# Performance work log

Hardware: AMD Instinct MI355X
Metric: run time of the kernel (lower is better)

Reference implementation:

```python
import jax, jax.numpy as jnp
import numpy as np

HID = 1024     # hidden_dim
HEADS = 8      # num_heads
HD = HID // HEADS  # head_dim = 128
MD = 8         # manifold_dim
L = 3          # num_layers
B, S = 8, 1024
EPS = 1e-7
BALL_MAX = 1.0 - 1e-5  # clamp inside Poincare ball (|curvature| = 1)


def expmap0(v):
    """Hyperbolic exponential map at origin, curvature -1 (Poincare ball)."""
    n = jnp.sqrt(jnp.sum(v * v, axis=-1, keepdims=True))
    n = jnp.maximum(n, EPS)
    return jnp.tanh(n) * v / n


def logmap0(y):
    """Hyperbolic logarithm map at origin, curvature -1 (Poincare ball)."""
    n = jnp.sqrt(jnp.sum(y * y, axis=-1, keepdims=True))
    n_c = jnp.clip(n, EPS, BALL_MAX)
    return jnp.arctanh(n_c) * y / n_c


def setup_inputs() -> dict:
    key = jax.random.key(0)
    ks = jax.random.split(key, 6)
    sc = 0.02
    return {
        "x": jax.random.normal(ks[0], (B, S, HID), dtype=jnp.float32),
        "W_qkv": jax.random.normal(ks[1], (HID, 3 * HID), dtype=jnp.float32) * sc,
        "b_qkv": jnp.zeros((3 * HID,), dtype=jnp.float32),
        "W_pinv": jax.random.normal(ks[2], (HID, MD), dtype=jnp.float32) * sc,
        "b_pinv": jnp.zeros((MD,), dtype=jnp.float32),
        "W_attn": jax.random.normal(ks[3], (L, MD, HID), dtype=jnp.float32) * sc,
        "b_attn": jnp.zeros((L, HID), dtype=jnp.float32),
        "W_out": jax.random.normal(ks[4], (HID, HID), dtype=jnp.float32) * sc,
        "b_out": jnp.zeros((HID,), dtype=jnp.float32),
    }


def reference(x, W_qkv, b_qkv, W_pinv, b_pinv, W_attn, b_attn, W_out, b_out):
    inv_sqrt_d = 1.0 / np.sqrt(HD).astype(np.float32)
    cur = x
    for l in range(L):
        qkv = jnp.einsum('bsh,hd->bsd', cur, W_qkv) + b_qkv  # [B,S,3*HID]
        q, k, v = jnp.split(qkv, 3, axis=-1)
        # [B,S,HID] -> [B,HEADS,S,HD]
        def heads(t):
            return t.reshape(B, S, HEADS, HD).transpose(0, 2, 1, 3)
        q, k, v = heads(q), heads(k), heads(v)
        # geometric 'flow': hyperbolic retraction of Q/K onto the Poincare ball
        # (parallel transport at the origin is identity)
        qf = expmap0(q)
        kf = expmap0(k)
        scores = jnp.einsum('bhqd,bhkd->bhqk', qf, kf) * inv_sqrt_d
        att = jax.nn.softmax(scores, axis=-1)
        o = jnp.einsum('bhqk,bhkd->bhqd', att, v)  # [B,H,S,HD]
        o = o.transpose(0, 2, 1, 3).reshape(B, S, HID)
        # project to manifold coords, then per-layer pattern projection back
        m = jnp.einsum('bsh,hm->bsm', o, W_pinv) + b_pinv           # [B,S,MD]
        upd = jnp.einsum('bsm,mh->bsh', m, W_attn[l]) + b_attn[l]   # [B,S,HID]
        cur = cur + upd
    return jnp.einsum('bsh,hd->bsd', cur, W_out) + b_out
```

## Files before the change

### kernel.cpp

```cpp
#include <hip/hip_runtime.h>
#include <hip/hip_bf16.h>
#include <hip/hip_fp8.h>
#include <cstdint>

typedef __hip_bfloat16 bf16;
typedef __bf16 b8 __attribute__((ext_vector_type(8)));
typedef float f4v __attribute__((ext_vector_type(4)));
typedef short s8v __attribute__((ext_vector_type(8)));
typedef int i8v __attribute__((ext_vector_type(8)));

#define DEVI static __device__ __forceinline__

DEVI void gload16(const void* g, void* l) {
  __builtin_amdgcn_global_load_lds(
      (const __attribute__((address_space(1))) void*)(uintptr_t)g,
      (__attribute__((address_space(3))) void*)(uint32_t)(uintptr_t)l,
      16, 0, 0);
}

DEVI f4v mfma_bf16(b8 a, b8 b, f4v c) {
  return __builtin_amdgcn_mfma_f32_16x16x32_bf16(a, b, c, 0, 0, 0);
}

DEVI f4v mfma_fp8(i8v a, i8v b, f4v c) {
  return __builtin_amdgcn_mfma_scale_f32_16x16x128_f8f6f4(
      a, b, c, 0, 0, 0, 0x7F7F7F7F, 0, 0x7F7F7F7F);
}

DEVI uint8_t to_fp8(float f) {
  __hip_fp8_e4m3 v(f);
  return v.__x;
}

__global__ void prep_kernel(const float* __restrict__ x, float* __restrict__ cur,
                            bf16* __restrict__ curb, uint8_t* __restrict__ curf8) {
  int i = (blockIdx.x * 256 + threadIdx.x) * 4;
  float4 v = *(const float4*)(x + i);
  *(float4*)(cur + i) = v;
  __hip_bfloat162 a, b;
  a.x = __float2bfloat16(v.x); a.y = __float2bfloat16(v.y);
  b.x = __float2bfloat16(v.z); b.y = __float2bfloat16(v.w);
  *(__hip_bfloat162*)(curb + i) = a;
  *(__hip_bfloat162*)(curb + i + 2) = b;
  uint32_t p = (uint32_t)to_fp8(v.x) | ((uint32_t)to_fp8(v.y) << 8) |
               ((uint32_t)to_fp8(v.z) << 16) | ((uint32_t)to_fp8(v.w) << 24);
  *(uint32_t*)(curf8 + i) = p;
}

__global__ void transpose_cast(const float* __restrict__ in, bf16* __restrict__ out,
                               int R, int C) {
  __shared__ float tile[32][33];
  int c0 = blockIdx.x * 32, r0 = blockIdx.y * 32;
  int tx = threadIdx.x & 31, ty = threadIdx.x >> 5;
  for (int rr = ty; rr < 32; rr += 8)
    tile[rr][tx] = in[(size_t)(r0 + rr) * C + c0 + tx];
  __syncthreads();
  for (int cc = ty; cc < 32; cc += 8)
    out[(size_t)(c0 + cc) * R + r0 + tx] = __float2bfloat16(tile[tx][cc]);
}

__global__ void transpose_cast_fp8(const float* __restrict__ in,
                                   uint8_t* __restrict__ out, int R, int C) {
  __shared__ float tile[32][33];
  int c0 = blockIdx.x * 32, r0 = blockIdx.y * 32;
  int tx = threadIdx.x & 31, ty = threadIdx.x >> 5;
  for (int rr = ty; rr < 32; rr += 8)
    tile[rr][tx] = in[(size_t)(r0 + rr) * C + c0 + tx];
  __syncthreads();
  for (int cc = ty; cc < 32; cc += 8)
    out[(size_t)(c0 + cc) * R + r0 + tx] = to_fp8(tile[tx][cc]);
}

__global__ __launch_bounds__(256, 3)
void gemm_qkv_fp8(const uint8_t* __restrict__ A, const uint8_t* __restrict__ Bt,
                  const float* __restrict__ bias, bf16* __restrict__ Qo,
                  bf16* __restrict__ Ko, bf16* __restrict__ Vto, int M, int N,
                  int K) {
  __shared__ uint8_t As[128 * 128];
  __shared__ uint8_t Bs[128 * 128];
  __shared__ float red[2][128];
  const int t = threadIdx.x;
  const int w = t >> 6, lane = t & 63;
  const int lm = lane & 15, qd = lane >> 4;
  const int m0 = blockIdx.x * 128, n0 = blockIdx.y * 128;
  const int wm = (w & 1) * 64, wn = (w >> 1) * 64;

  const uint8_t* Ag = A + (size_t)m0 * K;
  const uint8_t* Bg = Bt + (size_t)n0 * K;

  f4v acc[4][4];
  f4v zero = {0.f, 0.f, 0.f, 0.f};
#pragma unroll
  for (int i = 0; i < 4; i++)
#pragma unroll
    for (int j = 0; j < 4; j++) acc[i][j] = zero;

  for (int k0 = 0; k0 < K; k0 += 128) {
#pragma unroll
    for (int c = 0; c < 4; c++) {
      int s = c * 256 + t;
      int r = s >> 3;
      int kc = (s & 7) ^ (r & 7);
      gload16(Ag + (size_t)r * K + k0 + kc * 16, &As[s * 16]);
      gload16(Bg + (size_t)r * K + k0 + kc * 16, &Bs[s * 16]);
    }
    __syncthreads();
    i8v af[4], bfr[4];
#pragma unroll
    for (int tm = 0; tm < 4; tm++) {
      int row = wm + tm * 16 + lm;
      int ch = (qd * 2) ^ (row & 7);
      union { int4 q[2]; i8v v; } u;
      u.q[0] = *(const int4*)&As[row * 128 + ch * 16];
      u.q[1] = *(const int4*)&As[row * 128 + (ch ^ 1) * 16];
      af[tm] = u.v;
    }
#pragma unroll
    for (int tn = 0; tn < 4; tn++) {
      int row = wn + tn * 16 + lm;
      int ch = (qd * 2) ^ (row & 7);
      union { int4 q[2]; i8v v; } u;
      u.q[0] = *(const int4*)&Bs[row * 128 + ch * 16];
      u.q[1] = *(const int4*)&Bs[row * 128 + (ch ^ 1) * 16];
      bfr[tn] = u.v;
    }
    __builtin_amdgcn_s_setprio(1);
#pragma unroll
    for (int tm = 0; tm < 4; tm++)
#pragma unroll
      for (int tn = 0; tn < 4; tn++)
        acc[tm][tn] = mfma_fp8(af[tm], bfr[tn], acc[tm][tn]);
    __builtin_amdgcn_s_setprio(0);
    __syncthreads();
  }

  const int part = n0 >> 10;
  const int hh = (n0 >> 7) & 7;
  if (part == 2) {
#pragma unroll
    for (int tm = 0; tm < 4; tm++)
#pragma unroll
      for (int tn = 0; tn < 4; tn++) {
        int d = wn + tn * 16 + lm;
        float bv = bias[n0 + d];
        int row0 = m0 + wm + tm * 16 + qd * 4;
        int b = row0 >> 10, s0 = row0 & 1023;
        bf16 vt[4];
#pragma unroll
        for (int r = 0; r < 4; r++) vt[r] = __float2bfloat16(acc[tm][tn][r] + bv);
        *(ushort4*)&Vto[((size_t)(b * 8 + hh)) * 131072 + (size_t)d * 1024 + s0] =
            *(ushort4*)vt;
      }
  } else {
    float bvs[4];
#pragma unroll
    for (int tn = 0; tn < 4; tn++) bvs[tn] = bias[n0 + wn + tn * 16 + lm];
    float ss[4][4];
#pragma unroll
    for (int tm = 0; tm < 4; tm++)
#pragma unroll
      for (int r = 0; r < 4; r++) {
        float s = 0.f;
#pragma unroll
        for (int tn = 0; tn < 4; tn++) {
          float v = acc[tm][tn][r] + bvs[tn];
          s += v * v;
        }
#pragma unroll
        for (int off = 1; off < 16; off <<= 1) s += __shfl_xor(s, off, 64);
        ss[tm][r] = s;
      }
    if (lm == 0) {
#pragma unroll
      for (int tm = 0; tm < 4; tm++)
#pragma unroll
        for (int r = 0; r < 4; r++)
          red[w >> 1][wm + tm * 16 + qd * 4 + r] = ss[tm][r];
    }
    __syncthreads();
    const float qsc = (part == 0) ? 0.08838834764831845f : 1.0f;
    float scr[4][4];
#pragma unroll
    for (int tm = 0; tm < 4; tm++)
#pragma unroll
      for (int r = 0; r < 4; r++) {
        int row = wm + tm * 16 + qd * 4 + r;
        float tot = red[0][row] + red[1][row];
        float nrm = fmaxf(sqrtf(tot), 1e-7f);
        scr[tm][r] = tanhf(nrm) / nrm * qsc;
      }
    bf16* dst = (part == 0) ? Qo : Ko;
#pragma unroll
    for (int tm = 0; tm < 4; tm++)
#pragma unroll
      for (int tn = 0; tn < 4; tn++) {
        int d = wn + tn * 16 + lm;
        int row0 = m0 + wm + tm * 16 + qd * 4;
        int b = row0 >> 10, s0 = row0 & 1023;
#pragma unroll
        for (int r = 0; r < 4; r++)
          dst[(((size_t)(b * 8 + hh)) * 1024 + s0 + r) * 128 + d] =
              __float2bfloat16((acc[tm][tn][r] + bvs[tn]) * scr[tm][r]);
      }
  }
}

__global__ __launch_bounds__(256, 3)
void gemm_bt(const bf16* __restrict__ A, const bf16* __restrict__ Bt,
             const float* __restrict__ bias, float* __restrict__ Cf, int M, int N,
             int K) {
  __shared__ bf16 As[128 * 64];
  __shared__ bf16 Bs[128 * 64];
  const int t = threadIdx.x;
  const int w = t >> 6, lane = t & 63;
  const int lm = lane & 15, qd = lane >> 4;
  const int m0 = blockIdx.x * 128, n0 = blockIdx.y * 128;
  const int wm = (w & 1) * 64, wn = (w >> 1) * 64;

  const bf16* Ag = A + (size_t)m0 * K;
  const bf16* Bg = Bt + (size_t)n0 * K;

  f4v acc[4][4];
  f4v zero = {0.f, 0.f, 0.f, 0.f};
#pragma unroll
  for (int i = 0; i < 4; i++)
#pragma unroll
    for (int j = 0; j < 4; j++) acc[i][j] = zero;

  for (int k0 = 0; k0 < K; k0 += 64) {
#pragma unroll
    for (int c = 0; c < 4; c++) {
      int s = c * 256 + t;
      int r = s >> 3;
      int kc = (s & 7) ^ (r & 7);
      gload16(Ag + (size_t)r * K + k0 + kc * 8, &As[s * 8]);
      gload16(Bg + (size_t)r * K + k0 + kc * 8, &Bs[s * 8]);
    }
    __syncthreads();
#pragma unroll
    for (int ks = 0; ks < 2; ks++) {
      b8 af[4], bfr[4];
#pragma unroll
      for (int tm = 0; tm < 4; tm++) {
        int row = wm + tm * 16 + lm;
        int ch = (ks * 4 + qd) ^ (row & 7);
        af[tm] = *(const b8*)&As[row * 64 + ch * 8];
      }
#pragma unroll
      for (int tn = 0; tn < 4; tn++) {
        int row = wn + tn * 16 + lm;
        int ch = (ks * 4 + qd) ^ (row & 7);
        bfr[tn] = *(const b8*)&Bs[row * 64 + ch * 8];
      }
      __builtin_amdgcn_s_setprio(1);
#pragma unroll
      for (int tm = 0; tm < 4; tm++)
#pragma unroll
        for (int tn = 0; tn < 4; tn++)
          acc[tm][tn] = mfma_bf16(af[tm], bfr[tn], acc[tm][tn]);
      __builtin_amdgcn_s_setprio(0);
    }
    __syncthreads();
  }

#pragma unroll
  for (int tm = 0; tm < 4; tm++)
#pragma unroll
    for (int tn = 0; tn < 4; tn++) {
      int col = n0 + wn + tn * 16 + lm;
      float bv = bias[col];
#pragma unroll
      for (int r = 0; r < 4; r++) {
        int row = m0 + wm + tm * 16 + qd * 4 + r;
        Cf[(size_t)row * N + col] = acc[tm][tn][r] + bv;
      }
    }
}

__global__ __launch_bounds__(256, 2)
void attn_kernel(const bf16* __restrict__ Qf, const bf16* __restrict__ Kf,
                 const bf16* __restrict__ Vt, const float* __restrict__ Wpinv,
                 float* __restrict__ Mpart) {
  __shared__ bf16 smem[40960];
  bf16* Ps = smem + 32768;
  const int t = threadIdx.x, w = t >> 6, lane = t & 63;
  const int lm = lane & 15, qd = lane >> 4;
  const int bh = blockIdx.x, qt = blockIdx.y;
  const bf16* Qg = Qf + ((size_t)bh * 1024 + qt * 128) * 128;
  const bf16* Kg = Kf + (size_t)bh * 131072;
  const bf16* Vg = Vt + (size_t)bh * 131072;
  bf16* Pw = Ps + w * 2048;

  auto stage = [&](int kt, int b) {
    bf16* Ksb = smem + b * 16384;
    bf16* Vsb = Ksb + 8192;
#pragma unroll
    for (int c = 0; c < 4; c++) {
      int s = c * 256 + t;
      int r = s >> 4;
      int kc = (s & 15) ^ (r & 7);
      gload16(Kg + (size_t)(kt * 64 + r) * 128 + kc * 8, &Ksb[s * 8]);
      int rv = s >> 3;
      int kv = (s & 7) ^ (rv & 7);
      gload16(Vg + (size_t)rv * 1024 + kt * 64 + kv * 8, &Vsb[s * 8]);
    }
  };

  b8 qfr[2][4];
#pragma unroll
  for (int mt = 0; mt < 2; mt++)
#pragma unroll
    for (int ks = 0; ks < 4; ks++)
      qfr[mt][ks] =
          *(const b8*)(Qg + (size_t)(w * 32 + mt * 16 + lm) * 128 + ks * 32 + qd * 8);

  f4v o[2][8];
  f4v lacc[2];
  f4v zero = {0.f, 0.f, 0.f, 0.f};
#pragma unroll
  for (int mt = 0; mt < 2; mt++) {
    lacc[mt] = zero;
#pragma unroll
    for (int i = 0; i < 8; i++) o[mt][i] = zero;
  }
  union { s8v s; b8 b; } uo;
#pragma unroll
  for (int i = 0; i < 8; i++) uo.s[i] = 0x3F80;
  const b8 ones = uo.b;

  stage(0, 0);
  for (int kt = 0; kt < 16; kt++) {
    const int cb = kt & 1;
    if (kt < 15) {
      stage(kt + 1, cb ^ 1);
      asm volatile("s_waitcnt vmcnt(8)" ::: "memory");
    } else {
      asm volatile("s_waitcnt vmcnt(0)" ::: "memory");
    }
    __builtin_amdgcn_sched_barrier(0);
    __builtin_amdgcn_s_barrier();
    __builtin_amdgcn_sched_barrier(0);
    const bf16* Ks = smem + cb * 16384;
    const bf16* Vs = Ks + 8192;

    f4v sc[2][4];
#pragma unroll
    for (int mt = 0; mt < 2; mt++)
#pragma unroll
      for (int tn = 0; tn < 4; tn++) sc[mt][tn] = zero;
    __builtin_amdgcn_s_setprio(1);
#pragma unroll
    for (int tn = 0; tn < 4; tn++) {
      int krow = tn * 16 + lm;
#pragma unroll
      for (int ks = 0; ks < 4; ks++) {
        int ch = (ks * 4 + qd) ^ (krow & 7);
        b8 kfr = *(const b8*)&Ks[krow * 128 + ch * 8];
        sc[0][tn] = mfma_bf16(qfr[0][ks], kfr, sc[0][tn]);
        sc[1][tn] = mfma_bf16(qfr[1][ks], kfr, sc[1][tn]);
      }
    }
    __builtin_amdgcn_s_setprio(0);
#pragma unroll
    for (int mt = 0; mt < 2; mt++)
#pragma unroll
      for (int tn = 0; tn < 4; tn++)
#pragma unroll
        for (int r = 0; r < 4; r++) {
          int qi = mt * 16 + qd * 4 + r;
          int ch = (tn * 2 + (lm >> 3)) ^ ((qi >> 1) & 7);
          Pw[qi * 64 + ch * 8 + (lm & 7)] = __float2bfloat16(__expf(sc[mt][tn][r]));
        }

    b8 pa[2][2];
#pragma unroll
    for (int mt = 0; mt < 2; mt++)
#pragma unroll
      for (int kv2 = 0; kv2 < 2; kv2++) {
        int qi = mt * 16 + lm;
        int ch = (kv2 * 4 + qd) ^ ((lm >> 1) & 7);
        pa[mt][kv2] = *(const b8*)&Pw[qi * 64 + ch * 8];
      }
    __builtin_amdgcn_s_setprio(1);
#pragma unroll
    for (int mt = 0; mt < 2; mt++)
#pragma unroll
      for (int kv2 = 0; kv2 < 2; kv2++)
        lacc[mt] = mfma_bf16(pa[mt][kv2], ones, lacc[mt]);
#pragma unroll
    for (int tnd = 0; tnd < 8; tnd++) {
      int drow = tnd * 16 + lm;
#pragma unroll
      for (int kv2 = 0; kv2 < 2; kv2++) {
        int ch = (kv2 * 4 + qd) ^ (drow & 7);
        b8 vfr = *(const b8*)&Vs[drow * 64 + ch * 8];
#pragma unroll
        for (int mt = 0; mt < 2; mt++)
          o[mt][tnd] = mfma_bf16(pa[mt][kv2], vfr, o[mt][tnd]);
      }
    }
    __builtin_amdgcn_s_setprio(0);
    __builtin_amdgcn_sched_barrier(0);
    __builtin_amdgcn_s_barrier();
  }

  const int h = bh & 7;
  float wp[8][8];
#pragma unroll
  for (int tnd = 0; tnd < 8; tnd++) {
    const float* wr = Wpinv + (size_t)(h * 128 + tnd * 16 + lm) * 8;
    float4 wa = *(const float4*)wr;
    float4 wb = *(const float4*)(wr + 4);
    wp[tnd][0] = wa.x; wp[tnd][1] = wa.y; wp[tnd][2] = wa.z; wp[tnd][3] = wa.w;
    wp[tnd][4] = wb.x; wp[tnd][5] = wb.y; wp[tnd][6] = wb.z; wp[tnd][7] = wb.w;
  }
#pragma unroll
  for (int mt = 0; mt < 2; mt++) {
    float rinv[4];
#pragma unroll
    for (int r = 0; r < 4; r++) rinv[r] = 1.0f / lacc[mt][r];
#pragma unroll
    for (int r = 0; r < 4; r++) {
      float pm[8];
#pragma unroll
      for (int j = 0; j < 8; j++) pm[j] = 0.f;
#pragma unroll
      for (int tnd = 0; tnd < 8; tnd++) {
        float ov = o[mt][tnd][r] * rinv[r];
#pragma unroll
        for (int j = 0; j < 8; j++) pm[j] += ov * wp[tnd][j];
      }
#pragma unroll
      for (int j = 0; j < 8; j++) {
#pragma unroll
        for (int off = 1; off < 16; off <<= 1)
          pm[j] += __shfl_xor(pm[j], off, 64);
      }
      float sv = pm[0];
#pragma unroll
      for (int j = 1; j < 8; j++) sv = (lm == j) ? pm[j] : sv;
      if (lm < 8) {
        int sIdx = qt * 128 + w * 32 + mt * 16 + qd * 4 + r;
        Mpart[((size_t)bh * 1024 + sIdx) * 8 + lm] = sv;
      }
    }
  }
}

__global__ __launch_bounds__(256, 4)
void update_kernel(const float* __restrict__ Mpart, const float* __restrict__ bpinv,
                   const float* __restrict__ Wattn, const float* __restrict__ battn,
                   float* __restrict__ cur, bf16* __restrict__ curb,
                   uint8_t* __restrict__ curf8) {
  const int t = threadIdx.x, w = t >> 6, lane = t & 63;
  const int r0 = blockIdx.x * 8 + w * 2;
  const int hb = lane * 4;
  const int hh = lane >> 3, jj = lane & 7;

  float a0[8], a1[8];
  {
    const int b0 = r0 >> 10, s0 = r0 & 1023;
    float v0 = Mpart[(((size_t)b0 * 8 + hh) * 1024 + s0) * 8 + jj];
    float v1 = Mpart[(((size_t)b0 * 8 + hh) * 1024 + s0 + 1) * 8 + jj];
#pragma unroll
    for (int off = 8; off < 64; off <<= 1) {
      v0 += __shfl_xor(v0, off, 64);
      v1 += __shfl_xor(v1, off, 64);
    }
#pragma unroll
    for (int j = 0; j < 8; j++) {
      float bp = bpinv[j];
      a0[j] = __shfl(v0, j, 64) + bp;
      a1[j] = __shfl(v1, j, 64) + bp;
    }
  }

#pragma unroll
  for (int c = 0; c < 4; c++) {
    float4 bv = *(const float4*)(battn + c * 256 + hb);
    float u00 = bv.x, u01 = bv.y, u02 = bv.z, u03 = bv.w;
    float u10 = bv.x, u11 = bv.y, u12 = bv.z, u13 = bv.w;
#pragma unroll
    for (int j = 0; j < 8; j++) {
      float4 wv = *(const float4*)(Wattn + (size_t)j * 1024 + c * 256 + hb);
      u00 += a0[j] * wv.x; u01 += a0[j] * wv.y;
      u02 += a0[j] * wv.z; u03 += a0[j] * wv.w;
      u10 += a1[j] * wv.x; u11 += a1[j] * wv.y;
      u12 += a1[j] * wv.z; u13 += a1[j] * wv.w;
    }
    {
      float* cp = cur + (size_t)r0 * 1024 + c * 256 + hb;
      float4 c4 = *(float4*)cp;
      c4.x += u00; c4.y += u01; c4.z += u02; c4.w += u03;
      *(float4*)cp = c4;
      bf16 cb[4];
      cb[0] = __float2bfloat16(c4.x); cb[1] = __float2bfloat16(c4.y);
      cb[2] = __float2bfloat16(c4.z); cb[3] = __float2bfloat16(c4.w);
      *(ushort4*)(curb + (size_t)r0 * 1024 + c * 256 + hb) = *(ushort4*)cb;
      uint32_t p = (uint32_t)to_fp8(c4.x) | ((uint32_t)to_fp8(c4.y) << 8) |
                   ((uint32_t)to_fp8(c4.z) << 16) | ((uint32_t)to_fp8(c4.w) << 24);
      *(uint32_t*)(curf8 + (size_t)r0 * 1024 + c * 256 + hb) = p;
    }
    {
      float* cp = cur + (size_t)(r0 + 1) * 1024 + c * 256 + hb;
      float4 c4 = *(float4*)cp;
      c4.x += u10; c4.y += u11; c4.z += u12; c4.w += u13;
      *(float4*)cp = c4;
      bf16 cb[4];
      cb[0] = __float2bfloat16(c4.x); cb[1] = __float2bfloat16(c4.y);
      cb[2] = __float2bfloat16(c4.z); cb[3] = __float2bfloat16(c4.w);
      *(ushort4*)(curb + (size_t)(r0 + 1) * 1024 + c * 256 + hb) = *(ushort4*)cb;
      uint32_t p = (uint32_t)to_fp8(c4.x) | ((uint32_t)to_fp8(c4.y) << 8) |
                   ((uint32_t)to_fp8(c4.z) << 16) | ((uint32_t)to_fp8(c4.w) << 24);
      *(uint32_t*)(curf8 + (size_t)(r0 + 1) * 1024 + c * 256 + hb) = p;
    }
  }
}

extern "C" void kernel_launch(void* const* d_in, const int* in_sizes, int n_in,
                              void* d_out, int out_size, void* d_ws, size_t ws_size,
                              hipStream_t stream) {
  const float* x      = (const float*)d_in[0];
  const float* W_qkv  = (const float*)d_in[1];
  const float* b_qkv  = (const float*)d_in[2];
  const float* W_pinv = (const float*)d_in[3];
  const float* b_pinv = (const float*)d_in[4];
  const float* W_attn = (const float*)d_in[5];
  const float* b_attn = (const float*)d_in[6];
  const float* W_out  = (const float*)d_in[7];
  const float* b_out  = (const float*)d_in[8];

  char* ws = (char*)d_ws;
  size_t off = 0;
  auto alloc = [&](size_t bytes) -> void* {
    void* p = ws + off;
    off += (bytes + 255) & ~(size_t)255;
    return p;
  };
  float* cur     = (float*)alloc((size_t)8192 * 1024 * 4);
  bf16* curb     = (bf16*)alloc((size_t)8192 * 1024 * 2);
  uint8_t* curf8 = (uint8_t*)alloc((size_t)8192 * 1024);
  uint8_t* Wqkv8 = (uint8_t*)alloc((size_t)3072 * 1024);
  bf16* Woutt    = (bf16*)alloc((size_t)1024 * 1024 * 2);
  bf16* Q        = (bf16*)alloc((size_t)8192 * 1024 * 2);
  bf16* Kt       = (bf16*)alloc((size_t)8192 * 1024 * 2);
  bf16* Vt       = (bf16*)alloc((size_t)8192 * 1024 * 2);
  float* Mpart   = (float*)alloc((size_t)65536 * 8 * 4);
  (void)ws_size; (void)in_sizes; (void)n_in; (void)out_size;

  prep_kernel<<<8192, 256, 0, stream>>>(x, cur, curb, curf8);
  transpose_cast_fp8<<<dim3(96, 32), 256, 0, stream>>>(W_qkv, Wqkv8, 1024, 3072);
  transpose_cast<<<dim3(32, 32), 256, 0, stream>>>(W_out, Woutt, 1024, 1024);

  for (int l = 0; l < 3; l++) {
    gemm_qkv_fp8<<<dim3(64, 24), 256, 0, stream>>>(curf8, Wqkv8, b_qkv, Q, Kt, Vt,
                                                   8192, 3072, 1024);
    attn_kernel<<<dim3(64, 8), 256, 0, stream>>>(Q, Kt, Vt, W_pinv, Mpart);
    update_kernel<<<1024, 256, 0, stream>>>(Mpart, b_pinv,
                                            W_attn + (size_t)l * 8 * 1024,
                                            b_attn + (size_t)l * 1024, cur, curb,
                                            curf8);
  }
  gemm_bt<<<dim3(64, 8), 256, 0, stream>>>(curb, Woutt, b_out, (float*)d_out, 8192,
                                           1024, 1024);
}
```

Measured before the change: 450.7 us.

## Software-pipeline PV MFMAs one tile behind QK and drop trailing barrier

Restructures the attention inner loop so that the P·V MFMAs for tile kt-1 are issued alongside the QK^T MFMAs of tile kt. The P and V fragments are held in registers across iterations, and the leftover P·V is drained after the loop. The next tile's stage is now issued after the top barrier, with a full vmcnt(0) wait, and the end-of-loop barrier is removed. The aim is to overlap the exp/LDS-write latency with matrix work and to cut barriers. In exchange it raises register pressure through the 16 V fragments and changes the order of loads.

```diff
diff --git a/kernel.cpp b/kernel.cpp
--- a/kernel.cpp
+++ b/kernel.cpp
@@ -328,17 +328,17 @@
   for (int i = 0; i < 8; i++) uo.s[i] = 0x3F80;
   const b8 ones = uo.b;
 
+  b8 paP[2][2];
+  b8 vfP[8][2];
+
   stage(0, 0);
   for (int kt = 0; kt < 16; kt++) {
     const int cb = kt & 1;
-    if (kt < 15) {
-      stage(kt + 1, cb ^ 1);
-      asm volatile("s_waitcnt vmcnt(8)" ::: "memory");
-    } else {
-      asm volatile("s_waitcnt vmcnt(0)" ::: "memory");
-    }
+    asm volatile("s_waitcnt vmcnt(0)" ::: "memory");
     __builtin_amdgcn_sched_barrier(0);
     __builtin_amdgcn_s_barrier();
+    __builtin_amdgcn_sched_barrier(0);
+    if (kt < 15) stage(kt + 1, cb ^ 1);
     __builtin_amdgcn_sched_barrier(0);
     const bf16* Ks = smem + cb * 16384;
     const bf16* Vs = Ks + 8192;
@@ -360,7 +360,28 @@
         sc[1][tn] = mfma_bf16(qfr[1][ks], kfr, sc[1][tn]);
       }
     }
+    if (kt > 0) {
+#pragma unroll
+      for (int tnd = 0; tnd < 8; tnd++)
+#pragma unroll
+        for (int kv2 = 0; kv2 < 2; kv2++) {
+#pragma unroll
+          for (int mt = 0; mt < 2; mt++)
+            o[mt][tnd] = mfma_bf16(paP[mt][kv2], vfP[tnd][kv2], o[mt][tnd]);
+        }
+    }
     __builtin_amdgcn_s_setprio(0);
+
+#pragma unroll
+    for (int tnd = 0; tnd < 8; tnd++) {
+      int drow = tnd * 16 + lm;
+#pragma unroll
+      for (int kv2 = 0; kv2 < 2; kv2++) {
+        int ch = (kv2 * 4 + qd) ^ (drow & 7);
+        vfP[tnd][kv2] = *(const b8*)&Vs[drow * 64 + ch * 8];
+      }
+    }
+
 #pragma unroll
     for (int mt = 0; mt < 2; mt++)
 #pragma unroll
@@ -372,37 +393,36 @@
           Pw[qi * 64 + ch * 8 + (lm & 7)] = __float2bfloat16(__expf(sc[mt][tn][r]));
         }
 
-    b8 pa[2][2];
 #pragma unroll
     for (int mt = 0; mt < 2; mt++)
 #pragma unroll
       for (int kv2 = 0; kv2 < 2; kv2++) {
         int qi = mt * 16 + lm;
         int ch = (kv2 * 4 + qd) ^ ((lm >> 1) & 7);
-        pa[mt][kv2] = *(const b8*)&Pw[qi * 64 + ch * 8];
+        paP[mt][kv2] = *(const b8*)&Pw[qi * 64 + ch * 8];
       }
     __builtin_amdgcn_s_setprio(1);
 #pragma unroll
     for (int mt = 0; mt < 2; mt++)
 #pragma unroll
       for (int kv2 = 0; kv2 < 2; kv2++)
-        lacc[mt] = mfma_bf16(pa[mt][kv2], ones, lacc[mt]);
-#pragma unroll
-    for (int tnd = 0; tnd < 8; tnd++) {
-      int drow = tnd * 16 + lm;
-#pragma unroll
-      for (int kv2 = 0; kv2 < 2; kv2++) {
-        int ch = (kv2 * 4 + qd) ^ (drow & 7);
-        b8 vfr = *(const b8*)&Vs[drow * 64 + ch * 8];
-#pragma unroll
-        for (int mt = 0; mt < 2; mt++)
-          o[mt][tnd] = mfma_bf16(pa[mt][kv2], vfr, o[mt][tnd]);
-      }
-    }
+        lacc[mt] = mfma_bf16(paP[mt][kv2], ones, lacc[mt]);
     __builtin_amdgcn_s_setprio(0);
+
+    asm volatile("s_waitcnt lgkmcnt(0)" ::: "memory");
     __builtin_amdgcn_sched_barrier(0);
-    __builtin_amdgcn_s_barrier();
-  }
+  }
+
+  __builtin_amdgcn_s_setprio(1);
+#pragma unroll
+  for (int tnd = 0; tnd < 8; tnd++)
+#pragma unroll
+    for (int kv2 = 0; kv2 < 2; kv2++) {
+#pragma unroll
+      for (int mt = 0; mt < 2; mt++)
+        o[mt][tnd] = mfma_bf16(paP[mt][kv2], vfP[tnd][kv2], o[mt][tnd]);
+    }
+  __builtin_amdgcn_s_setprio(0);
 
   const int h = bh & 7;
   float wp[8][8];
```

Measured after the change: 462.2 us. 2.5% more time.
